# Performance work log

Hardware: AMD Instinct MI355X
Metric: run time of the kernel (lower is better)

## Reference

```python
import jax, jax.numpy as jnp
import numpy as np


def _pool2(x):
    # 2x2 max pool, stride 2 (matches F.max_pool2d(x, 2))
    b, c, h, w = x.shape
    return x.reshape(b, c, h // 2, 2, w // 2, 2).max(axis=(3, 5))


def setup_inputs() -> dict:
    key = jax.random.key(0)
    ks = jax.random.split(key, 6)
    B, C, H, W = 16, 512, 64, 64
    x = jax.random.normal(ks[0], (B, C, H, W), dtype=jnp.float32)
    scale = 0.02
    theta_w = jax.random.normal(ks[1], (C // 8, C), dtype=jnp.float32) * scale
    phi_w = jax.random.normal(ks[2], (C // 8, C), dtype=jnp.float32) * scale
    g_w = jax.random.normal(ks[3], (C // 2, C), dtype=jnp.float32) * scale
    o_w = jax.random.normal(ks[4], (C, C // 2), dtype=jnp.float32) * scale
    # original inits gamma=0; use a nonzero value so output depends on attention path
    gamma = jax.random.normal(ks[5], (), dtype=jnp.float32) * 0.5
    return {"x": x, "theta_w": theta_w, "phi_w": phi_w, "g_w": g_w, "o_w": o_w, "gamma": gamma}


def reference(x, theta_w, phi_w, g_w, o_w, gamma):
    B, C, H, W = x.shape
    HW = H * W
    # 1x1 convs == channel GEMMs
    theta = jnp.einsum('bchw,kc->bkhw', x, theta_w).reshape(B, C // 8, HW).transpose(0, 2, 1)  # [B, HW, C/8]
    phi = _pool2(jnp.einsum('bchw,kc->bkhw', x, phi_w)).reshape(B, C // 8, HW // 4)            # [B, C/8, HW/4]
    beta = jax.nn.softmax(jnp.einsum('bnk,bkm->bnm', theta, phi), axis=-1)                     # [B, HW, HW/4]
    g = _pool2(jnp.einsum('bchw,kc->bkhw', x, g_w)).reshape(B, C // 2, HW // 4)                # [B, C/2, HW/4]
    # g.bmm(beta^T): contract over pooled positions m -> [B, C/2, HW]
    o_in = jnp.einsum('bcm,bnm->bcn', g, beta).reshape(B, C // 2, H, W)
    o = jnp.einsum('bchw,kc->bkhw', o_in, o_w)                                                 # [B, C, H, W]
    return gamma * o + x
```

## Files before the change

### kernel.cpp

```cpp
#include <hip/hip_runtime.h>

#define B_   16
#define C_   512
#define HW_  4096
#define M_   1024
#define TPAD 136

typedef __attribute__((ext_vector_type(8))) short bf16x8;
typedef __attribute__((ext_vector_type(4))) float f32x4;

static __device__ __forceinline__ unsigned short f2bf(float f) {
    union { float f; unsigned u; } v; v.f = f;
    unsigned r = v.u + 0x7fffu + ((v.u >> 16) & 1u);
    return (unsigned short)(r >> 16);
}
static __device__ __forceinline__ float bf2f(unsigned short h) {
    union { unsigned u; float f; } v; v.u = ((unsigned)h) << 16;
    return v.f;
}
static __device__ __forceinline__ void gload_lds16(const void* g, void* l) {
    __builtin_amdgcn_global_load_lds(
        (const __attribute__((address_space(1))) unsigned int*)g,
        (__attribute__((address_space(3))) unsigned int*)l, 16, 0, 0);
}
static __device__ __forceinline__ int fb(int row) { return (row ^ (row >> 2)) & 7; }

__global__ __launch_bounds__(256) void k_weights(
    const float* __restrict__ thw, const float* __restrict__ phw,
    const float* __restrict__ gw,  const float* __restrict__ ow,
    unsigned short* __restrict__ Wb, unsigned short* __restrict__ oWb,
    unsigned short* __restrict__ g_p) {
    int i = blockIdx.x * 256 + threadIdx.x;
    if (i < 32768)        Wb[i] = f2bf(thw[i]);
    else if (i < 65536)   Wb[i] = f2bf(phw[i - 32768]);
    else if (i < 196608)  Wb[i] = f2bf(gw[i - 65536]);
    else if (i < 327680)  oWb[i - 196608] = f2bf(ow[i - 196608]);
    else if (i < 589824) {
        int i2 = i - 327680;
        int b = i2 >> 14;
        int r = (i2 >> 10) & 15;
        int m = i2 & 1023;
        g_p[((size_t)b * 272 + 256 + r) * M_ + m] =
            (r == 0) ? (unsigned short)0x3F80u : (unsigned short)0;
    }
}

__global__ __launch_bounds__(256, 4) void k_proj(
    const float* __restrict__ x, const unsigned short* __restrict__ Wb,
    unsigned short* __restrict__ theta_n, unsigned short* __restrict__ phi_p,
    unsigned short* __restrict__ g_p) {
    __shared__ unsigned short smem[128 * TPAD];
    unsigned short* As = smem;
    unsigned short* Bs = smem + 8192;

    int b = blockIdx.z, mt = blockIdx.y, bx = blockIdx.x;
    int hw0 = bx * 128;
    int tid = threadIdx.x, w = tid >> 6, lane = tid & 63;
    int l15 = lane & 15, q = lane >> 4;
    int wr = w >> 1, wc = w & 1;

    const unsigned short* Ab = Wb + (size_t)(mt * 128) * 512;
    const float* xb = x + (size_t)b * C_ * HW_ + hw0;
    int trow = tid >> 3, tch = tid & 7;
    int hg4 = (tid & 31) * 4;
    int kq2 = (tid >> 5) * 2;

    f32x4 acc[4][4] = {};
    for (int ks = 0; ks < 8; ks++) {
        int k0 = ks * 64;
        if (ks) __syncthreads();
#pragma unroll
        for (int i = 0; i < 4; i++) {
            int row = i * 32 + trow;
            int ch = tch ^ (row & 7);
            gload_lds16(Ab + (size_t)row * 512 + k0 + ch * 8, &As[(i * 256 + w * 64) * 8]);
        }
#pragma unroll
        for (int it = 0; it < 2; it++) {
            int kg = kq2 + it;
            const float* xs = xb + (size_t)(k0 + kg * 4) * HW_ + hg4;
            float4 r0 = *reinterpret_cast<const float4*>(xs);
            float4 r1 = *reinterpret_cast<const float4*>(xs + HW_);
            float4 r2 = *reinterpret_cast<const float4*>(xs + 2 * HW_);
            float4 r3 = *reinterpret_cast<const float4*>(xs + 3 * HW_);
            const float* p0 = (const float*)&r0; const float* p1 = (const float*)&r1;
            const float* p2 = (const float*)&r2; const float* p3 = (const float*)&r3;
#pragma unroll
            for (int t = 0; t < 4; t++) {
                int row = hg4 + t;
                int ch = (kg >> 1) ^ fb(row);
                ushort4 u;
                u.x = f2bf(p0[t]); u.y = f2bf(p1[t]);
                u.z = f2bf(p2[t]); u.w = f2bf(p3[t]);
                *reinterpret_cast<ushort4*>(&Bs[row * 64 + ch * 8 + (kg & 1) * 4]) = u;
            }
        }
        __syncthreads();
#pragma unroll
        for (int kk = 0; kk < 2; kk++) {
            bf16x8 af[4], bfr[4];
#pragma unroll
            for (int mi = 0; mi < 4; mi++) {
                int row = wr * 64 + mi * 16 + l15;
                int ch = (kk * 4 + q) ^ (row & 7);
                af[mi] = *(const bf16x8*)&As[row * 64 + ch * 8];
            }
#pragma unroll
            for (int ni = 0; ni < 4; ni++) {
                int row = wc * 64 + ni * 16 + l15;
                int ch = (kk * 4 + q) ^ fb(row);
                bfr[ni] = *(const bf16x8*)&Bs[row * 64 + ch * 8];
            }
#pragma unroll
            for (int mi = 0; mi < 4; mi++)
#pragma unroll
                for (int ni = 0; ni < 4; ni++)
                    acc[mi][ni] = __builtin_amdgcn_mfma_f32_16x16x32_bf16(
                        af[mi], bfr[ni], acc[mi][ni], 0, 0, 0);
        }
    }

    __syncthreads();
#pragma unroll
    for (int mi = 0; mi < 4; mi++)
#pragma unroll
        for (int ni = 0; ni < 4; ni++) {
            int col = wc * 64 + ni * 16 + l15;
            int row = wr * 64 + mi * 16 + q * 4;
            ushort4 u;
            u.x = f2bf(acc[mi][ni][0]); u.y = f2bf(acc[mi][ni][1]);
            u.z = f2bf(acc[mi][ni][2]); u.w = f2bf(acc[mi][ni][3]);
            *reinterpret_cast<ushort4*>(&smem[col * TPAD + row]) = u;
        }
    __syncthreads();

    if (mt == 0) {
        int hw_l = tid >> 1, kh = (tid & 1) * 32;
        const unsigned short* srcp = &smem[hw_l * TPAD + kh];
        unsigned short* dstp = theta_n + ((size_t)b * HW_ + hw0 + hw_l) * 64 + kh;
#pragma unroll
        for (int i = 0; i < 4; i++)
            *reinterpret_cast<uint4*>(dstp + i * 8) =
                *reinterpret_cast<const uint4*>(srcp + i * 8);
        int pc = tid & 63, mg = tid >> 6;
#pragma unroll
        for (int j = 0; j < 8; j++) {
            int m_l = mg * 8 + j, w_ = m_l * 2;
            float v0 = bf2f(smem[(w_)      * TPAD + 64 + pc]);
            float v1 = bf2f(smem[(w_ + 1)  * TPAD + 64 + pc]);
            float v2 = bf2f(smem[(64 + w_) * TPAD + 64 + pc]);
            float v3 = bf2f(smem[(65 + w_) * TPAD + 64 + pc]);
            float v = fmaxf(fmaxf(v0, v1), fmaxf(v2, v3));
            phi_p[((size_t)b * M_ + bx * 32 + m_l) * 64 + pc] = f2bf(v);
        }
    } else {
        int lr = tid & 127, half = tid >> 7;
        int gc = (mt - 1) * 128 + lr;
        unsigned short* dst = g_p + ((size_t)b * 272 + gc) * M_ + bx * 32 + half * 16;
        unsigned short tmp[16];
#pragma unroll
        for (int i = 0; i < 16; i++) {
            int w_ = (half * 16 + i) * 2;
            float v0 = bf2f(smem[(w_)      * TPAD + lr]);
            float v1 = bf2f(smem[(w_ + 1)  * TPAD + lr]);
            float v2 = bf2f(smem[(64 + w_) * TPAD + lr]);
            float v3 = bf2f(smem[(65 + w_) * TPAD + lr]);
            tmp[i] = f2bf(fmaxf(fmaxf(v0, v1), fmaxf(v2, v3)));
        }
#pragma unroll
        for (int i = 0; i < 4; i++)
            *reinterpret_cast<ushort4*>(dst + i * 4) =
                *reinterpret_cast<const ushort4*>(&tmp[i * 4]);
    }
}

__global__ __launch_bounds__(512, 4) void k_attn(
    const unsigned short* __restrict__ theta_n, const unsigned short* __restrict__ phi_p,
    const unsigned short* __restrict__ g_p, unsigned short* __restrict__ o_in) {
    __shared__ unsigned short phi_s[64 * 64];
    __shared__ unsigned short g_s[272 * 64];
    __shared__ unsigned short p_lds[8][16][88];

    int b = blockIdx.y, n0 = blockIdx.x * 128;
    int tid = threadIdx.x, w = tid >> 6, lane = tid & 63;
    int l15 = lane & 15, q = lane >> 4;
    int nw = n0 + w * 16;

    const unsigned short* th = theta_n + ((size_t)b * HW_ + nw + l15) * 64 + q * 8;
    bf16x8 a0 = *(const bf16x8*)(th);
    bf16x8 a1 = *(const bf16x8*)(th + 32);

    const unsigned short* phib = phi_p + (size_t)b * M_ * 64;
    const unsigned short* gb   = g_p   + (size_t)b * 272 * M_;

    int sw = l15 & 7;

    f32x4 acc[17] = {};
    for (int mc = 0; mc < 16; mc++) {
        int m0 = mc * 64;
        __syncthreads();
        {
            int p = tid;
            int row = p >> 3, ch = (p & 7) ^ (row & 7);
            gload_lds16(phib + (size_t)(m0 + row) * 64 + ch * 8, &phi_s[w * 512]);
        }
#pragma unroll
        for (int it = 0; it < 5; it++) {
            int s = w + it * 8;
            if (s < 34) {
                int row = s * 8 + (lane >> 3);
                int ch = (lane & 7) ^ (row & 7);
                gload_lds16(gb + (size_t)row * M_ + m0 + ch * 8, &g_s[s * 512]);
            }
        }
        __syncthreads();

#pragma unroll
        for (int f = 0; f < 4; f++) {
            const unsigned short* pr = &phi_s[(f * 16 + l15) * 64];
            bf16x8 b0 = *(const bf16x8*)(pr + (q ^ sw) * 8);
            bf16x8 b1 = *(const bf16x8*)(pr + ((q + 4) ^ sw) * 8);
            f32x4 s = {};
            s = __builtin_amdgcn_mfma_f32_16x16x32_bf16(a0, b0, s, 0, 0, 0);
            s = __builtin_amdgcn_mfma_f32_16x16x32_bf16(a1, b1, s, 0, 0, 0);
#pragma unroll
            for (int j = 0; j < 4; j++)
                p_lds[w][q * 4 + j][f * 16 + l15] = f2bf(__expf(s[j]));
        }
        bf16x8 p0 = *(const bf16x8*)&p_lds[w][l15][q * 8];
        bf16x8 p1 = *(const bf16x8*)&p_lds[w][l15][32 + q * 8];
#pragma unroll
        for (int cf = 0; cf < 17; cf++) {
            const unsigned short* gr = &g_s[(cf * 16 + l15) * 64];
            bf16x8 g0 = *(const bf16x8*)(gr + (q ^ sw) * 8);
            bf16x8 g1 = *(const bf16x8*)(gr + ((q + 4) ^ sw) * 8);
            acc[cf] = __builtin_amdgcn_mfma_f32_16x16x32_bf16(p0, g0, acc[cf], 0, 0, 0);
            acc[cf] = __builtin_amdgcn_mfma_f32_16x16x32_bf16(p1, g1, acc[cf], 0, 0, 0);
        }
    }

    float dinv[4];
#pragma unroll
    for (int j = 0; j < 4; j++) {
        float d = __shfl(acc[16][j], (lane & 48), 64);
        dinv[j] = 1.0f / d;
    }
#pragma unroll
    for (int cf = 0; cf < 16; cf++)
#pragma unroll
        for (int j = 0; j < 4; j++)
            o_in[((size_t)b * HW_ + nw + q * 4 + j) * 256 + cf * 16 + l15] =
                f2bf(acc[cf][j] * dinv[j]);
}

__global__ __launch_bounds__(256, 4) void k_oproj(
    const unsigned short* __restrict__ o_in, const unsigned short* __restrict__ oWb,
    const float* __restrict__ x, const float* __restrict__ gamma_p,
    float* __restrict__ out) {
    __shared__ unsigned short smem[128 * TPAD];
    unsigned short* As = smem;
    unsigned short* Bs = smem + 8192;

    int b = blockIdx.z, mt = blockIdx.y, hw0 = blockIdx.x * 128;
    int tid = threadIdx.x, w = tid >> 6, lane = tid & 63;
    int l15 = lane & 15, q = lane >> 4;
    int wr = w >> 1, wc = w & 1;

    const unsigned short* Ab = oWb + (size_t)(mt * 128) * 256;
    const unsigned short* Bb = o_in + ((size_t)b * HW_ + hw0) * 256;
    int trow = tid >> 3, tch = tid & 7;

    f32x4 acc[4][4] = {};
    for (int ks = 0; ks < 4; ks++) {
        int k0 = ks * 64;
        if (ks) __syncthreads();
#pragma unroll
        for (int i = 0; i < 4; i++) {
            int row = i * 32 + trow;
            int ch = tch ^ (row & 7);
            gload_lds16(Ab + (size_t)row * 256 + k0 + ch * 8, &As[(i * 256 + w * 64) * 8]);
        }
#pragma unroll
        for (int i = 0; i < 4; i++) {
            int row = i * 32 + trow;
            int ch = tch ^ (row & 7);
            gload_lds16(Bb + (size_t)row * 256 + k0 + ch * 8, &Bs[(i * 256 + w * 64) * 8]);
        }
        __syncthreads();
#pragma unroll
        for (int kk = 0; kk < 2; kk++) {
            bf16x8 af[4], bfr[4];
#pragma unroll
            for (int mi = 0; mi < 4; mi++) {
                int row = wr * 64 + mi * 16 + l15;
                int ch = (kk * 4 + q) ^ (row & 7);
                af[mi] = *(const bf16x8*)&As[row * 64 + ch * 8];
            }
#pragma unroll
            for (int ni = 0; ni < 4; ni++) {
                int row = wc * 64 + ni * 16 + l15;
                int ch = (kk * 4 + q) ^ (row & 7);
                bfr[ni] = *(const bf16x8*)&Bs[row * 64 + ch * 8];
            }
#pragma unroll
            for (int mi = 0; mi < 4; mi++)
#pragma unroll
                for (int ni = 0; ni < 4; ni++)
                    acc[mi][ni] = __builtin_amdgcn_mfma_f32_16x16x32_bf16(
                        af[mi], bfr[ni], acc[mi][ni], 0, 0, 0);
        }
    }

    __syncthreads();
#pragma unroll
    for (int mi = 0; mi < 4; mi++)
#pragma unroll
        for (int ni = 0; ni < 4; ni++) {
            int col = wc * 64 + ni * 16 + l15;
            int rb = wr * 64 + mi * 16 + q * 4;
#pragma unroll
            for (int j = 0; j < 4; j++)
                smem[(rb + j) * TPAD + col] = f2bf(acc[mi][ni][j]);
        }
    __syncthreads();

    float gam = *gamma_p;
    int sub = tid >> 5, p32 = tid & 31;
#pragma unroll
    for (int p = 0; p < 16; p++) {
        int row = p * 8 + sub;
        ushort4 v = *reinterpret_cast<const ushort4*>(&smem[row * TPAD + p32 * 4]);
        size_t idx = ((size_t)b * C_ + mt * 128 + row) * HW_ + hw0 + p32 * 4;
        float4 xv = *reinterpret_cast<const float4*>(x + idx);
        float4 o;
        o.x = gam * bf2f(v.x) + xv.x;
        o.y = gam * bf2f(v.y) + xv.y;
        o.z = gam * bf2f(v.z) + xv.z;
        o.w = gam * bf2f(v.w) + xv.w;
        *reinterpret_cast<float4*>(out + idx) = o;
    }
}

extern "C" void kernel_launch(void* const* d_in, const int* in_sizes, int n_in,
                              void* d_out, int out_size, void* d_ws, size_t ws_size,
                              hipStream_t stream) {
    const float* x     = (const float*)d_in[0];
    const float* thw   = (const float*)d_in[1];
    const float* phw   = (const float*)d_in[2];
    const float* gw    = (const float*)d_in[3];
    const float* ow    = (const float*)d_in[4];
    const float* gamma = (const float*)d_in[5];
    float* out = (float*)d_out;

    char* ws = (char*)d_ws;
    unsigned short* Wb   = (unsigned short*)(ws + 0);
    unsigned short* oWb  = (unsigned short*)(ws + 393216);
    unsigned short* oin  = (unsigned short*)(ws + 655360);
    unsigned short* thn  = (unsigned short*)(ws + 34209792);
    unsigned short* phip = (unsigned short*)(ws + 42598400);
    unsigned short* gp   = (unsigned short*)(ws + 44695552);

    hipLaunchKernelGGL(k_weights, dim3(2304), dim3(256), 0, stream, thw, phw, gw, ow, Wb, oWb, gp);
    hipLaunchKernelGGL(k_proj, dim3(32, 3, 16), dim3(256), 0, stream, x, Wb, thn, phip, gp);
    hipLaunchKernelGGL(k_attn, dim3(32, 16), dim3(512), 0, stream, thn, phip, gp, oin);
    hipLaunchKernelGGL(k_oproj, dim3(32, 4, 16), dim3(256), 0, stream, oin, oWb, x, gamma, out);
}
```

Before: 198.9 us.

## Double-buffer x tile in k_proj and read weights directly from global

Restructures the projection GEMM main loop so the next k-slice of x is prefetched into registers while MFMAs run on the current LDS buffer, then written to a second LDS buffer. This uses one barrier per iteration instead of two. Weight fragments are now loaded straight from global memory (L2-resident) instead of being staged through LDS with global_load_lds. The extra prefetch registers lead to lowering launch bounds from 4 to 2 waves per SIMD, which reduces occupancy.

```diff
diff --git a/kernel.cpp b/kernel.cpp
--- a/kernel.cpp
+++ b/kernel.cpp
@@ -45,13 +45,13 @@
     }
 }
 
-__global__ __launch_bounds__(256, 4) void k_proj(
+__global__ __launch_bounds__(256, 2) void k_proj(
     const float* __restrict__ x, const unsigned short* __restrict__ Wb,
     unsigned short* __restrict__ theta_n, unsigned short* __restrict__ phi_p,
     unsigned short* __restrict__ g_p) {
     __shared__ unsigned short smem[128 * TPAD];
-    unsigned short* As = smem;
-    unsigned short* Bs = smem + 8192;
+    unsigned short* Bs0 = smem;
+    unsigned short* Bs1 = smem + 8192;
 
     int b = blockIdx.z, mt = blockIdx.y, bx = blockIdx.x;
     int hw0 = bx * 128;
@@ -61,64 +61,78 @@
 
     const unsigned short* Ab = Wb + (size_t)(mt * 128) * 512;
     const float* xb = x + (size_t)b * C_ * HW_ + hw0;
-    int trow = tid >> 3, tch = tid & 7;
     int hg4 = (tid & 31) * 4;
     int kq2 = (tid >> 5) * 2;
 
+    float4 breg[8];
+
+#define LOADB(k0v)                                                             \
+    _Pragma("unroll")                                                          \
+    for (int it = 0; it < 2; it++) {                                           \
+        int kg = kq2 + it;                                                     \
+        const float* xs = xb + (size_t)((k0v) + kg * 4) * HW_ + hg4;           \
+        breg[it * 4 + 0] = *reinterpret_cast<const float4*>(xs);               \
+        breg[it * 4 + 1] = *reinterpret_cast<const float4*>(xs + HW_);         \
+        breg[it * 4 + 2] = *reinterpret_cast<const float4*>(xs + 2 * HW_);     \
+        breg[it * 4 + 3] = *reinterpret_cast<const float4*>(xs + 3 * HW_);     \
+    }
+
+#define WRITEB(dst)                                                            \
+    _Pragma("unroll")                                                          \
+    for (int it = 0; it < 2; it++) {                                           \
+        int kg = kq2 + it;                                                     \
+        _Pragma("unroll")                                                      \
+        for (int t = 0; t < 4; t++) {                                          \
+            int row = hg4 + t;                                                 \
+            int ch = (kg >> 1) ^ fb(row);                                      \
+            ushort4 u;                                                         \
+            u.x = f2bf(((const float*)&breg[it * 4 + 0])[t]);                  \
+            u.y = f2bf(((const float*)&breg[it * 4 + 1])[t]);                  \
+            u.z = f2bf(((const float*)&breg[it * 4 + 2])[t]);                  \
+            u.w = f2bf(((const float*)&breg[it * 4 + 3])[t]);                  \
+            *reinterpret_cast<ushort4*>(&(dst)[row * 64 + ch * 8 + (kg & 1) * 4]) = u; \
+        }                                                                      \
+    }
+
+    LOADB(0);
+    WRITEB(Bs0);
+
     f32x4 acc[4][4] = {};
+#pragma unroll
     for (int ks = 0; ks < 8; ks++) {
         int k0 = ks * 64;
-        if (ks) __syncthreads();
-#pragma unroll
-        for (int i = 0; i < 4; i++) {
-            int row = i * 32 + trow;
-            int ch = tch ^ (row & 7);
-            gload_lds16(Ab + (size_t)row * 512 + k0 + ch * 8, &As[(i * 256 + w * 64) * 8]);
-        }
-#pragma unroll
-        for (int it = 0; it < 2; it++) {
-            int kg = kq2 + it;
-            const float* xs = xb + (size_t)(k0 + kg * 4) * HW_ + hg4;
-            float4 r0 = *reinterpret_cast<const float4*>(xs);
-            float4 r1 = *reinterpret_cast<const float4*>(xs + HW_);
-            float4 r2 = *reinterpret_cast<const float4*>(xs + 2 * HW_);
-            float4 r3 = *reinterpret_cast<const float4*>(xs + 3 * HW_);
-            const float* p0 = (const float*)&r0; const float* p1 = (const float*)&r1;
-            const float* p2 = (const float*)&r2; const float* p3 = (const float*)&r3;
-#pragma unroll
-            for (int t = 0; t < 4; t++) {
-                int row = hg4 + t;
-                int ch = (kg >> 1) ^ fb(row);
-                ushort4 u;
-                u.x = f2bf(p0[t]); u.y = f2bf(p1[t]);
-                u.z = f2bf(p2[t]); u.w = f2bf(p3[t]);
-                *reinterpret_cast<ushort4*>(&Bs[row * 64 + ch * 8 + (kg & 1) * 4]) = u;
-            }
-        }
+        unsigned short* cur = (ks & 1) ? Bs1 : Bs0;
+        unsigned short* nxt = (ks & 1) ? Bs0 : Bs1;
         __syncthreads();
-#pragma unroll
-        for (int kk = 0; kk < 2; kk++) {
-            bf16x8 af[4], bfr[4];
+        bf16x8 af[2][4];
+#pragma unroll
+        for (int kk = 0; kk < 2; kk++)
 #pragma unroll
             for (int mi = 0; mi < 4; mi++) {
                 int row = wr * 64 + mi * 16 + l15;
-                int ch = (kk * 4 + q) ^ (row & 7);
-                af[mi] = *(const bf16x8*)&As[row * 64 + ch * 8];
-            }
+                af[kk][mi] = *(const bf16x8*)(Ab + (size_t)row * 512 + k0 + kk * 32 + q * 8);
+            }
+        if (ks < 7) { LOADB(k0 + 64); }
+#pragma unroll
+        for (int kk = 0; kk < 2; kk++) {
+            bf16x8 bfr[4];
 #pragma unroll
             for (int ni = 0; ni < 4; ni++) {
                 int row = wc * 64 + ni * 16 + l15;
                 int ch = (kk * 4 + q) ^ fb(row);
-                bfr[ni] = *(const bf16x8*)&Bs[row * 64 + ch * 8];
+                bfr[ni] = *(const bf16x8*)&cur[row * 64 + ch * 8];
             }
 #pragma unroll
             for (int mi = 0; mi < 4; mi++)
 #pragma unroll
                 for (int ni = 0; ni < 4; ni++)
                     acc[mi][ni] = __builtin_amdgcn_mfma_f32_16x16x32_bf16(
-                        af[mi], bfr[ni], acc[mi][ni], 0, 0, 0);
-        }
-    }
+                        af[kk][mi], bfr[ni], acc[mi][ni], 0, 0, 0);
+        }
+        if (ks < 7) { WRITEB(nxt); }
+    }
+#undef LOADB
+#undef WRITEB
 
     __syncthreads();
 #pragma unroll
```

Measured after the change: 189.1 us. -4.9%, faster.
